# Optimization experiments

Measured on AMD Instinct MI355X. Metric: run time of the kernel, lower is better.

## Reference

```python
import jax, jax.numpy as jnp
import numpy as np

N, M, D, P = 4096, 8192, 512, 4
TEMP = 0.1  # SimCLR temperature


def setup_inputs() -> dict:
    key = jax.random.key(0)
    k1, k2, k3, k4 = jax.random.split(key, 4)
    queries = jax.random.normal(k1, (N, D), dtype=jnp.float32)
    keys = jax.random.normal(k2, (M, D), dtype=jnp.float32)
    # positives in lower half, ignores in upper half -> disjoint, no all--inf rows
    positive_indices = jax.random.randint(k3, (N, P), 0, M // 2)
    ignore_indices = jax.random.randint(k4, (N, P), M // 2, M)
    return dict(queries=queries, keys=keys,
                positive_indices=positive_indices, ignore_indices=ignore_indices)


def reference(queries, keys, positive_indices, ignore_indices):
    n, m = queries.shape[0], keys.shape[0]
    # score_fn = dot-product similarity, divided by temperature -> [N, M]
    scores = jnp.matmul(queries, keys.T) / TEMP
    rows = jnp.arange(n)[:, None]
    # scatter per-row index lists into boolean masks (duplicates collapse, as in torch)
    pos_mask = jnp.zeros((n, m), dtype=bool).at[rows, positive_indices].set(True)
    ign_mask = jnp.zeros((n, m), dtype=bool).at[rows, ignore_indices].set(True)
    neg_inf = jnp.array(-jnp.inf, dtype=scores.dtype)
    scores_m = jnp.where(ign_mask, neg_inf, scores)  # masked_fill(ignore, -inf)
    # scatter_logsumexp over positives == row-wise logsumexp restricted to pos_mask
    pos_lse = jax.nn.logsumexp(jnp.where(pos_mask, scores_m, neg_inf), axis=1)
    logp = pos_lse - jax.nn.logsumexp(scores_m, axis=1)
    loss = -jnp.sum(logp)
    preds = jnp.argmax(scores_m, axis=1)  # [N]
    corrects = jnp.any(positive_indices == preds[:, None], axis=1)  # [N] bool
    return (loss, corrects)
```

## Files before the change

### kernel.cpp

```cpp
#include <hip/hip_runtime.h>
#include <math.h>

#define N_Q 4096
#define M_K 8192
#define D_DIM 512
#define P_IDX 4
#define INV_TEMP 10.0f

#define NCHUNK 256

typedef __attribute__((ext_vector_type(8))) _Float16 f16x8;
typedef __attribute__((ext_vector_type(16))) float f32x16;

__global__ __launch_bounds__(256)
void pack_f16(const float* __restrict__ Q, const float* __restrict__ K,
              _Float16* __restrict__ Pq, _Float16* __restrict__ Pk,
              int qunits, int totunits)
{
    const int wunit = blockIdx.x * 4 + (threadIdx.x >> 6);
    if (wunit >= totunits) return;
    const bool isq = (wunit < qunits);
    const int u = isq ? wunit : wunit - qunits;
    const float* X = isq ? Q : K;
    _Float16* P = isq ? Pq : Pk;
    const float scale = isq ? INV_TEMP : 1.0f;
    const int rb = u >> 5, ks = u & 31;
    const int lane = threadIdx.x & 63;
    const int hi = lane >> 5, lx = lane & 31;
    const int row = rb * 32 + lx;
    const float4* src = (const float4*)(X + (size_t)row * D_DIM + ks * 16 + hi * 8);
    float4 v0 = src[0], v1 = src[1];
    f16x8 o;
    o[0] = (_Float16)(v0.x * scale); o[1] = (_Float16)(v0.y * scale);
    o[2] = (_Float16)(v0.z * scale); o[3] = (_Float16)(v0.w * scale);
    o[4] = (_Float16)(v1.x * scale); o[5] = (_Float16)(v1.y * scale);
    o[6] = (_Float16)(v1.z * scale); o[7] = (_Float16)(v1.w * scale);
    ((f16x8*)P)[(size_t)u * 64 + lane] = o;
}

__global__ __launch_bounds__(256, 4)
void scores_mfma(const _Float16* __restrict__ Qp, const _Float16* __restrict__ Kp,
                 const int* __restrict__ ign, float4* __restrict__ part)
{
    const int tid = threadIdx.x;
    const int lane = tid & 63;
    const int wave = tid >> 6;
    const int wr = wave >> 1, wc = wave & 1;
    const int hi = lane >> 5, lx = lane & 31;
    const int bx = blockIdx.x;
    const int by = blockIdx.y;

    const f16x8* Kp8 = (const f16x8*)Kp;
    const f16x8* Qp8 = (const f16x8*)Qp;
    const f16x8* A0p = Kp8 + ((size_t)(bx * 4 + wr * 2 + 0) * 32) * 64 + lane;
    const f16x8* A1p = Kp8 + ((size_t)(bx * 4 + wr * 2 + 1) * 32) * 64 + lane;
    const f16x8* B0p = Qp8 + ((size_t)(by * 4 + wc * 2 + 0) * 32) * 64 + lane;
    const f16x8* B1p = Qp8 + ((size_t)(by * 4 + wc * 2 + 1) * 32) * 64 + lane;

    f32x16 acc[2][2];
#pragma unroll
    for (int i = 0; i < 2; ++i)
#pragma unroll
        for (int j = 0; j < 2; ++j) acc[i][j] = (f32x16)0.f;

    f16x8 pA0 = A0p[0],  pA1 = A1p[0],  pB0 = B0p[0],  pB1 = B1p[0];
    f16x8 qA0 = A0p[64], qA1 = A1p[64], qB0 = B0p[64], qB1 = B1p[64];

    for (int ks = 0; ks < 32; ks += 2) {
        __builtin_amdgcn_s_setprio(1);
        acc[0][0] = __builtin_amdgcn_mfma_f32_32x32x16_f16(pA0, pB0, acc[0][0], 0, 0, 0);
        acc[0][1] = __builtin_amdgcn_mfma_f32_32x32x16_f16(pA0, pB1, acc[0][1], 0, 0, 0);
        acc[1][0] = __builtin_amdgcn_mfma_f32_32x32x16_f16(pA1, pB0, acc[1][0], 0, 0, 0);
        acc[1][1] = __builtin_amdgcn_mfma_f32_32x32x16_f16(pA1, pB1, acc[1][1], 0, 0, 0);
        __builtin_amdgcn_s_setprio(0);
        if (ks + 2 < 32) {
            const int o = (ks + 2) * 64;
            pA0 = A0p[o]; pA1 = A1p[o]; pB0 = B0p[o]; pB1 = B1p[o];
        }
        __builtin_amdgcn_s_setprio(1);
        acc[0][0] = __builtin_amdgcn_mfma_f32_32x32x16_f16(qA0, qB0, acc[0][0], 0, 0, 0);
        acc[0][1] = __builtin_amdgcn_mfma_f32_32x32x16_f16(qA0, qB1, acc[0][1], 0, 0, 0);
        acc[1][0] = __builtin_amdgcn_mfma_f32_32x32x16_f16(qA1, qB0, acc[1][0], 0, 0, 0);
        acc[1][1] = __builtin_amdgcn_mfma_f32_32x32x16_f16(qA1, qB1, acc[1][1], 0, 0, 0);
        __builtin_amdgcn_s_setprio(0);
        if (ks + 3 < 32) {
            const int o = (ks + 3) * 64;
            qA0 = A0p[o]; qA1 = A1p[o]; qB0 = B0p[o]; qB1 = B1p[o];
        }
    }

    const int kbase = bx * 128 + wr * 64 + 4 * hi;
    const int chunk = bx * 4 + wr * 2 + hi;
#pragma unroll
    for (int j = 0; j < 2; ++j) {
        const int qrow = by * 128 + wc * 64 + j * 32 + lx;
        const int4 ig = ((const int4*)ign)[qrow];
        float bm = -INFINITY; int bi = 0x7fffffff;
#pragma unroll
        for (int i = 0; i < 2; ++i) {
#pragma unroll
            for (int r = 0; r < 16; ++r) {
                const int col = kbase + i * 32 + (r & 3) + 8 * (r >> 2);
                float x = acc[i][j][r];
                if (col == ig.x || col == ig.y || col == ig.z || col == ig.w)
                    x = -INFINITY;
                acc[i][j][r] = x;
                if (x > bm || (x == bm && col < bi)) { bm = x; bi = col; }
            }
        }
        float se = 0.f;
#pragma unroll
        for (int i = 0; i < 2; ++i)
#pragma unroll
            for (int r = 0; r < 16; ++r)
                se += __expf(acc[i][j][r] - bm);
        part[(size_t)qrow * NCHUNK + chunk] =
            make_float4(bm, se, __int_as_float(bi), 0.f);
    }
}

__global__ __launch_bounds__(64)
void combine_kernel(const float4* __restrict__ part,
                    const float* __restrict__ Q, const float* __restrict__ K,
                    const int* __restrict__ pos,
                    float* __restrict__ logp, float* __restrict__ corrects)
{
    const int row = blockIdx.x;
    const int lane = threadIdx.x;

    float4 p0 = part[(size_t)row * NCHUNK + lane];
    float m = p0.x, s = p0.y, av = p0.x;
    int ai = __float_as_int(p0.z);
#pragma unroll
    for (int k = 1; k < 4; ++k) {
        float4 p = part[(size_t)row * NCHUNK + k * 64 + lane];
        int oi = __float_as_int(p.z);
        float nm = fmaxf(m, p.x);
        s = s * expf(m - nm) + p.y * expf(p.x - nm);
        m = nm;
        if (p.x > av || (p.x == av && oi < ai)) { av = p.x; ai = oi; }
    }

#pragma unroll
    for (int off = 32; off >= 1; off >>= 1) {
        float om = __shfl_xor(m, off);
        float os = __shfl_xor(s, off);
        float oav = __shfl_xor(av, off);
        int oi = __shfl_xor(ai, off);
        float nm = fmaxf(m, om);
        s = s * expf(m - nm) + os * expf(om - nm);
        m = nm;
        if (oav > av || (oav == av && oi < ai)) { av = oav; ai = oi; }
    }
    float lse = m + logf(s);

    int pi[4];
#pragma unroll
    for (int p = 0; p < 4; ++p) pi[p] = pos[row * P_IDX + p];

    const float4* q4 = (const float4*)(Q + (size_t)row * D_DIM);
    float4 qa = q4[lane * 2], qb = q4[lane * 2 + 1];
    float d[4];
#pragma unroll
    for (int p = 0; p < 4; ++p) {
        const float4* k4 = (const float4*)(K + (size_t)pi[p] * D_DIM);
        float4 ka = k4[lane * 2], kb = k4[lane * 2 + 1];
        d[p] = qa.x * ka.x + qa.y * ka.y + qa.z * ka.z + qa.w * ka.w
             + qb.x * kb.x + qb.y * kb.y + qb.z * kb.z + qb.w * kb.w;
    }
#pragma unroll
    for (int off = 32; off >= 1; off >>= 1) {
#pragma unroll
        for (int p = 0; p < 4; ++p) d[p] += __shfl_xor(d[p], off);
    }

    if (lane == 0) {
        float ps[4];
#pragma unroll
        for (int p = 0; p < 4; ++p) ps[p] = d[p] * INV_TEMP;
        const bool v1 = (pi[1] != pi[0]);
        const bool v2 = (pi[2] != pi[0]) && (pi[2] != pi[1]);
        const bool v3 = (pi[3] != pi[0]) && (pi[3] != pi[1]) && (pi[3] != pi[2]);
        float pm = ps[0];
        if (v1) pm = fmaxf(pm, ps[1]);
        if (v2) pm = fmaxf(pm, ps[2]);
        if (v3) pm = fmaxf(pm, ps[3]);
        float pse = expf(ps[0] - pm);
        if (v1) pse += expf(ps[1] - pm);
        if (v2) pse += expf(ps[2] - pm);
        if (v3) pse += expf(ps[3] - pm);
        float pos_lse = pm + logf(pse);
        logp[row] = pos_lse - lse;
        bool corr = (ai == pi[0]) || (ai == pi[1]) || (ai == pi[2]) || (ai == pi[3]);
        corrects[row] = corr ? 1.0f : 0.0f;
    }
}

__global__ __launch_bounds__(256)
void loss_kernel(const float* __restrict__ logp, float* __restrict__ out)
{
    __shared__ float sm[256];
    const int t = threadIdx.x;
    float s = 0.f;
    for (int i = t; i < N_Q; i += 256) s += logp[i];
    sm[t] = s;
    __syncthreads();
    for (int off = 128; off >= 1; off >>= 1) {
        if (t < off) sm[t] += sm[t + off];
        __syncthreads();
    }
    if (t == 0) out[0] = -sm[0];
}

extern "C" void kernel_launch(void* const* d_in, const int* in_sizes, int n_in,
                              void* d_out, int out_size, void* d_ws, size_t ws_size,
                              hipStream_t stream)
{
    const float* Q = (const float*)d_in[0];
    const float* K = (const float*)d_in[1];
    const int* pos = (const int*)d_in[2];
    const int* ign = (const int*)d_in[3];
    float* out = (float*)d_out;

    _Float16* Qp = (_Float16*)d_ws;
    _Float16* Kp = Qp + (size_t)N_Q * D_DIM;
    float4* part = (float4*)(Kp + (size_t)M_K * D_DIM);
    float* logp = (float*)(part + (size_t)N_Q * NCHUNK);

    const int qunits = N_Q / 32 * 32;
    const int totunits = qunits + M_K / 32 * 32;
    pack_f16<<<totunits / 4, 256, 0, stream>>>(Q, K, Qp, Kp, qunits, totunits);

    dim3 gridA(M_K / 128, N_Q / 128);
    scores_mfma<<<gridA, 256, 0, stream>>>(Qp, Kp, ign, part);
    combine_kernel<<<N_Q, 64, 0, stream>>>(part, Q, K, pos, logp, out + 1);
    loss_kernel<<<1, 256, 0, stream>>>(logp, out);
}
```

Baseline: 75.48 us.

## Enlarge MFMA tile to 2x4 per wave and pack four rows per combine block

Each wave in the score GEMM now computes a 64x128 output tile (2 key blocks by 4 query blocks) instead of 64x64, halving the number of query-dimension blocks and raising operand reuse per global load. The occupancy hint on launch bounds is dropped to allow the larger accumulator and prefetch register footprint. The combine kernel is also restructured to process four rows per 256-thread block rather than one row per 64-thread block, reducing block launch count. Register pressure rises substantially, which may lower occupancy and latency hiding for the direct-from-global operand loads.

```diff
diff --git a/kernel.cpp b/kernel.cpp
--- a/kernel.cpp
+++ b/kernel.cpp
@@ -38,7 +38,7 @@
     ((f16x8*)P)[(size_t)u * 64 + lane] = o;
 }
 
-__global__ __launch_bounds__(256, 4)
+__global__ __launch_bounds__(256)
 void scores_mfma(const _Float16* __restrict__ Qp, const _Float16* __restrict__ Kp,
                  const int* __restrict__ ign, float4* __restrict__ part)
 {
@@ -52,48 +52,63 @@
 
     const f16x8* Kp8 = (const f16x8*)Kp;
     const f16x8* Qp8 = (const f16x8*)Qp;
-    const f16x8* A0p = Kp8 + ((size_t)(bx * 4 + wr * 2 + 0) * 32) * 64 + lane;
-    const f16x8* A1p = Kp8 + ((size_t)(bx * 4 + wr * 2 + 1) * 32) * 64 + lane;
-    const f16x8* B0p = Qp8 + ((size_t)(by * 4 + wc * 2 + 0) * 32) * 64 + lane;
-    const f16x8* B1p = Qp8 + ((size_t)(by * 4 + wc * 2 + 1) * 32) * 64 + lane;
-
-    f32x16 acc[2][2];
+    const f16x8* Ap[2];
+    const f16x8* Bp[4];
 #pragma unroll
     for (int i = 0; i < 2; ++i)
-#pragma unroll
-        for (int j = 0; j < 2; ++j) acc[i][j] = (f32x16)0.f;
-
-    f16x8 pA0 = A0p[0],  pA1 = A1p[0],  pB0 = B0p[0],  pB1 = B1p[0];
-    f16x8 qA0 = A0p[64], qA1 = A1p[64], qB0 = B0p[64], qB1 = B1p[64];
+        Ap[i] = Kp8 + ((size_t)(bx * 4 + wr * 2 + i) * 32) * 64 + lane;
+#pragma unroll
+    for (int j = 0; j < 4; ++j)
+        Bp[j] = Qp8 + ((size_t)(by * 8 + wc * 4 + j) * 32) * 64 + lane;
+
+    f32x16 acc[2][4];
+#pragma unroll
+    for (int i = 0; i < 2; ++i)
+#pragma unroll
+        for (int j = 0; j < 4; ++j) acc[i][j] = (f32x16)0.f;
+
+    f16x8 pA[2], pB[4], sA[2], sB[4];
+#pragma unroll
+    for (int i = 0; i < 2; ++i) { pA[i] = Ap[i][0]; sA[i] = Ap[i][64]; }
+#pragma unroll
+    for (int j = 0; j < 4; ++j) { pB[j] = Bp[j][0]; sB[j] = Bp[j][64]; }
 
     for (int ks = 0; ks < 32; ks += 2) {
         __builtin_amdgcn_s_setprio(1);
-        acc[0][0] = __builtin_amdgcn_mfma_f32_32x32x16_f16(pA0, pB0, acc[0][0], 0, 0, 0);
-        acc[0][1] = __builtin_amdgcn_mfma_f32_32x32x16_f16(pA0, pB1, acc[0][1], 0, 0, 0);
-        acc[1][0] = __builtin_amdgcn_mfma_f32_32x32x16_f16(pA1, pB0, acc[1][0], 0, 0, 0);
-        acc[1][1] = __builtin_amdgcn_mfma_f32_32x32x16_f16(pA1, pB1, acc[1][1], 0, 0, 0);
+#pragma unroll
+        for (int i = 0; i < 2; ++i)
+#pragma unroll
+            for (int j = 0; j < 4; ++j)
+                acc[i][j] = __builtin_amdgcn_mfma_f32_32x32x16_f16(pA[i], pB[j], acc[i][j], 0, 0, 0);
         __builtin_amdgcn_s_setprio(0);
         if (ks + 2 < 32) {
             const int o = (ks + 2) * 64;
-            pA0 = A0p[o]; pA1 = A1p[o]; pB0 = B0p[o]; pB1 = B1p[o];
+#pragma unroll
+            for (int i = 0; i < 2; ++i) pA[i] = Ap[i][o];
+#pragma unroll
+            for (int j = 0; j < 4; ++j) pB[j] = Bp[j][o];
         }
         __builtin_amdgcn_s_setprio(1);
-        acc[0][0] = __builtin_amdgcn_mfma_f32_32x32x16_f16(qA0, qB0, acc[0][0], 0, 0, 0);
-        acc[0][1] = __builtin_amdgcn_mfma_f32_32x32x16_f16(qA0, qB1, acc[0][1], 0, 0, 0);
-        acc[1][0] = __builtin_amdgcn_mfma_f32_32x32x16_f16(qA1, qB0, acc[1][0], 0, 0, 0);
-        acc[1][1] = __builtin_amdgcn_mfma_f32_32x32x16_f16(qA1, qB1, acc[1][1], 0, 0, 0);
+#pragma unroll
+        for (int i = 0; i < 2; ++i)
+#pragma unroll
+            for (int j = 0; j < 4; ++j)
+                acc[i][j] = __builtin_amdgcn_mfma_f32_32x32x16_f16(sA[i], sB[j], acc[i][j], 0, 0, 0);
         __builtin_amdgcn_s_setprio(0);
         if (ks + 3 < 32) {
             const int o = (ks + 3) * 64;
-            qA0 = A0p[o]; qA1 = A1p[o]; qB0 = B0p[o]; qB1 = B1p[o];
+#pragma unroll
+            for (int i = 0; i < 2; ++i) sA[i] = Ap[i][o];
+#pragma unroll
+            for (int j = 0; j < 4; ++j) sB[j] = Bp[j][o];
         }
     }
 
     const int kbase = bx * 128 + wr * 64 + 4 * hi;
     const int chunk = bx * 4 + wr * 2 + hi;
 #pragma unroll
-    for (int j = 0; j < 2; ++j) {
-        const int qrow = by * 128 + wc * 64 + j * 32 + lx;
+    for (int j = 0; j < 4; ++j) {
+        const int qrow = by * 256 + wc * 128 + j * 32 + lx;
         const int4 ig = ((const int4*)ign)[qrow];
         float bm = -INFINITY; int bi = 0x7fffffff;
 #pragma unroll
@@ -119,14 +134,14 @@
     }
 }
 
-__global__ __launch_bounds__(64)
+__global__ __launch_bounds__(256)
 void combine_kernel(const float4* __restrict__ part,
                     const float* __restrict__ Q, const float* __restrict__ K,
                     const int* __restrict__ pos,
                     float* __restrict__ logp, float* __restrict__ corrects)
 {
-    const int row = blockIdx.x;
-    const int lane = threadIdx.x;
+    const int row = blockIdx.x * 4 + (threadIdx.x >> 6);
+    const int lane = threadIdx.x & 63;
 
     float4 p0 = part[(size_t)row * NCHUNK + lane];
     float m = p0.x, s = p0.y, av = p0.x;
@@ -231,8 +246,8 @@
     const int totunits = qunits + M_K / 32 * 32;
     pack_f16<<<totunits / 4, 256, 0, stream>>>(Q, K, Qp, Kp, qunits, totunits);
 
-    dim3 gridA(M_K / 128, N_Q / 128);
+    dim3 gridA(M_K / 128, N_Q / 256);
     scores_mfma<<<gridA, 256, 0, stream>>>(Qp, Kp, ign, part);
-    combine_kernel<<<N_Q, 64, 0, stream>>>(part, Q, K, pos, logp, out + 1);
+    combine_kernel<<<N_Q / 4, 256, 0, stream>>>(part, Q, K, pos, logp, out + 1);
     loss_kernel<<<1, 256, 0, stream>>>(logp, out);
 }
```

Result: slower. 83.36 us (+10.4%).
